# Performance work log

Measured on AMD Instinct MI355X. Metric: run time of the kernel, lower is better.

The kernel has to match this reference:

```python
import jax, jax.numpy as jnp
import numpy as np
import math

B, S, HID, NH = 4, 2048, 1024, 16
HD = HID // NH  # head dim = 64


def setup_inputs() -> dict:
    key = jax.random.key(0)
    ks = jax.random.split(key, 8)
    sc = 0.02
    return {
        "x": jax.random.normal(ks[0], (B, S, HID), dtype=jnp.float32),
        "att_mask": jnp.zeros((B, 1, 1, S), dtype=jnp.float32),
        "Wq": jax.random.normal(ks[1], (HID, HID), dtype=jnp.float32) * sc,
        "bq": jax.random.normal(ks[2], (HID,), dtype=jnp.float32) * sc,
        "Wk": jax.random.normal(ks[3], (HID, HID), dtype=jnp.float32) * sc,
        "bk": jax.random.normal(ks[4], (HID,), dtype=jnp.float32) * sc,
        "Wv": jax.random.normal(ks[5], (HID, HID), dtype=jnp.float32) * sc,
        "bv": jax.random.normal(ks[6], (HID,), dtype=jnp.float32) * sc,
    }


def reference(x, att_mask, Wq, bq, Wk, bk, Wv, bv):
    # quant_mode=False path: QuantLinear acts as a plain affine projection
    # (the running min/max stats only calibrate `scale`, which is unused in
    # the float path), and IntSoftmax reduces to a standard softmax.
    q = x @ Wq.T + bq  # [B,S,HID]
    k = x @ Wk.T + bk
    v = x @ Wv.T + bv
    # split heads: [B,S,HID] -> [B,NH,S,HD]
    q = q.reshape(B, S, NH, HD).transpose(0, 2, 1, 3)
    k = k.reshape(B, S, NH, HD).transpose(0, 2, 1, 3)
    v = v.reshape(B, S, NH, HD).transpose(0, 2, 1, 3)
    scores = jnp.einsum("bhqd,bhkd->bhqk", q, k) / math.sqrt(HD) + att_mask
    probs = jax.nn.softmax(scores, axis=-1)  # [B,NH,S,S]
    ctx = jnp.einsum("bhqk,bhkd->bhqd", probs, v)  # [B,NH,S,HD]
    return ctx.transpose(0, 2, 1, 3).reshape(B, S, HID)
```

## Files before the change

### kernel.cpp

```cpp
#include <hip/hip_runtime.h>
#include <hip/hip_bf16.h>
#include <cstdint>
#include <cstddef>

#define BB   4
#define SS   2048
#define HIDD 1024
#define NHH  16
#define HDD  64
#define MM   (BB*SS)
#define L2E  1.4426950408889634f
#define SH4  5.770780163555854f

typedef __bf16    bf16x8 __attribute__((ext_vector_type(8)));
typedef float     f32x4  __attribute__((ext_vector_type(4)));
typedef _Float16  half4  __attribute__((ext_vector_type(4)));
typedef _Float16  half8  __attribute__((ext_vector_type(8)));
typedef _Float16  half2v __attribute__((ext_vector_type(2)));
typedef unsigned  u32x4  __attribute__((ext_vector_type(4)));

__device__ __forceinline__ unsigned short f2b(float f) {
    unsigned u = __builtin_bit_cast(unsigned, f);
    return (unsigned short)((u + 0x7FFFu + ((u >> 16) & 1u)) >> 16);
}

__device__ __forceinline__ half2v pkrtz(float a, float b) {
    return __builtin_bit_cast(half2v, __builtin_amdgcn_cvt_pkrtz(a, b));
}

__device__ __forceinline__ unsigned pkrtz_u(float a, float b) {
    return __builtin_bit_cast(unsigned, __builtin_amdgcn_cvt_pkrtz(a, b));
}

__device__ __forceinline__ void gl_lds16(const void* g, void* l) {
    __builtin_amdgcn_global_load_lds(
        (const __attribute__((address_space(1))) void*)g,
        (__attribute__((address_space(3))) void*)l, 16, 0, 0);
}

#define NX4 (MM * HIDD / 4)
#define NW4 (HIDD * HIDD / 4)
__global__ __launch_bounds__(256) void cvt_all(
    const float* __restrict__ x,  const float* __restrict__ wq,
    const float* __restrict__ wk, const float* __restrict__ wv,
    unsigned short* __restrict__ xb, unsigned short* __restrict__ wb)
{
    int i = blockIdx.x * 256 + threadIdx.x;
    const float* src; unsigned short* dst; int off;
    if (i < NX4) { src = x; dst = xb; off = i; }
    else {
        int j = i - NX4;
        int w = j >> 18;
        off = j & (NW4 - 1);
        src = (w == 0) ? wq : (w == 1) ? wk : wv;
        dst = wb + (size_t)w * HIDD * HIDD;
    }
    float4 v = reinterpret_cast<const float4*>(src)[off];
    ushort4 o;
    o.x = f2b(v.x); o.y = f2b(v.y); o.z = f2b(v.z); o.w = f2b(v.w);
    reinterpret_cast<ushort4*>(dst)[off] = o;
}

__global__ __launch_bounds__(256, 3) void qkv_gemm(
    const unsigned short* __restrict__ xb,
    const unsigned short* __restrict__ wb,
    const float* __restrict__ bq, const float* __restrict__ bk, const float* __restrict__ bv,
    unsigned short* __restrict__ Qb, unsigned short* __restrict__ Kb,
    _Float16* __restrict__ Vtb)
{
    __shared__ unsigned short lA[128 * 64];
    __shared__ unsigned short lB[128 * 64];

    const int tid  = threadIdx.x;
    const int wave = tid >> 6, lane = tid & 63;
    const int lh   = lane & 15, quad = lane >> 4;
    const int l7   = lh & 7;
    const int m0   = blockIdx.x * 128;
    const int opn  = blockIdx.y;
    const int op   = opn >> 3;
    const int n0   = (opn & 7) * 128;
    const unsigned short* W = wb + (size_t)op * HIDD * HIDD;
    const float* bias = (op == 0) ? bq : (op == 1) ? bk : bv;

    f32x4 acc[4][4];
#pragma unroll
    for (int i = 0; i < 4; i++)
#pragma unroll
        for (int j = 0; j < 4; j++) acc[i][j] = f32x4{0.f, 0.f, 0.f, 0.f};

    const int wm = wave & 1, wn = wave >> 1;
    const unsigned short* srcA = (op == 2) ? lA : lB;
    const unsigned short* srcB = (op == 2) ? lB : lA;
    const int offA = (op == 2) ? wm : wn;
    const int offB = (op == 2) ? wn : wm;

    const int srow = tid >> 3;
    const int sg   = tid & 7;

    for (int k0 = 0; k0 < HIDD; k0 += 64) {
#pragma unroll
        for (int rr = 0; rr < 4; rr++) {
            const int row = srow + rr * 32;
            const int gcol = k0 + ((sg ^ (row & 7)) << 3);
            gl_lds16(&xb[(size_t)(m0 + row) * HIDD + gcol], &lA[row * 64 + sg * 8]);
            gl_lds16(&W [(size_t)(n0 + row) * HIDD + gcol], &lB[row * 64 + sg * 8]);
        }
        __syncthreads();

#pragma unroll
        for (int kk = 0; kk < 2; kk++) {
            bf16x8 aF[4], bF[4];
#pragma unroll
            for (int i = 0; i < 4; i++) {
                const int row = offA * 64 + i * 16 + lh;
                aF[i] = *reinterpret_cast<const bf16x8*>(
                    &srcA[row * 64 + (((kk * 4 + quad) ^ l7) << 3)]);
            }
#pragma unroll
            for (int j = 0; j < 4; j++) {
                const int row = offB * 64 + j * 16 + lh;
                bF[j] = *reinterpret_cast<const bf16x8*>(
                    &srcB[row * 64 + (((kk * 4 + quad) ^ l7) << 3)]);
            }
#pragma unroll
            for (int i = 0; i < 4; i++)
#pragma unroll
                for (int j = 0; j < 4; j++)
                    acc[i][j] = __builtin_amdgcn_mfma_f32_16x16x32_bf16(aF[i], bF[j], acc[i][j], 0, 0, 0);
        }
        __syncthreads();
    }

    if (op == 2) {
#pragma unroll
        for (int j = 0; j < 4; j++) {
            const int n = n0 + offB * 64 + j * 16 + lh;
            const float bvv = bias[n];
            const int h = n >> 6, d = n & 63;
#pragma unroll
            for (int i = 0; i < 4; i++) {
                const int mrow = m0 + offA * 64 + i * 16 + quad * 4;
                const int b_ = mrow >> 11, s_ = mrow & 2047;
                half2v h01 = pkrtz(acc[i][j][0] + bvv, acc[i][j][1] + bvv);
                half2v h23 = pkrtz(acc[i][j][2] + bvv, acc[i][j][3] + bvv);
                half4 hv; hv[0] = h01[0]; hv[1] = h01[1]; hv[2] = h23[0]; hv[3] = h23[1];
                size_t a = ((size_t)(b_ * NHH + h) * HDD + d) * SS + s_;
                *reinterpret_cast<half4*>(&Vtb[a]) = hv;
            }
        }
    } else {
        const float qs = (op == 0) ? (0.125f * L2E) : 1.0f;
        unsigned short* dst = (op == 0) ? Qb : Kb;
#pragma unroll
        for (int i = 0; i < 4; i++) {
            const int nb = n0 + offA * 64 + i * 16 + quad * 4;
            const float4 bb = *reinterpret_cast<const float4*>(&bias[nb]);
            const int h = nb >> 6, d = nb & 63;
#pragma unroll
            for (int j = 0; j < 4; j++) {
                const int m = m0 + offB * 64 + j * 16 + lh;
                const int b_ = m >> 11, s_ = m & 2047;
                ushort4 o;
                o.x = f2b((acc[i][j][0] + bb.x) * qs);
                o.y = f2b((acc[i][j][1] + bb.y) * qs);
                o.z = f2b((acc[i][j][2] + bb.z) * qs);
                o.w = f2b((acc[i][j][3] + bb.w) * qs);
                *reinterpret_cast<ushort4*>(
                    &dst[((size_t)(b_ * NHH + h) * SS + s_) * HDD + d]) = o;
            }
        }
    }
}

__global__ __launch_bounds__(256, 4) void attn_kernel(
    const unsigned short* __restrict__ Qb,
    const unsigned short* __restrict__ Kb,
    const _Float16* __restrict__ Vtb,
    const float* __restrict__ mask,
    float* __restrict__ out)
{
    __shared__ unsigned short lK[2][64 * 64];
    __shared__ _Float16      lV[2][64 * 64];
    __shared__ float         lmm[SS];

    const int tid  = threadIdx.x;
    const int wave = tid >> 6, lane = tid & 63;
    const int lh   = lane & 15, quad = lane >> 4;
    const int l7   = lh & 7;
    const int bh = blockIdx.x, qt = blockIdx.y;
    const int b = bh >> 4, h = bh & 15;
    const unsigned short* Qh = Qb  + (size_t)bh * SS * HDD;
    const unsigned short* Kh = Kb  + (size_t)bh * SS * HDD;
    const _Float16*       Vh = Vtb + (size_t)bh * HDD * SS;
    const float* mk = mask + (size_t)b * SS;
    const int q0 = qt * 128;

    bf16x8 qF[2][2];
#pragma unroll
    for (int i = 0; i < 2; i++)
#pragma unroll
        for (int kk = 0; kk < 2; kk++)
            qF[i][kk] = *reinterpret_cast<const bf16x8*>(
                &Qh[(size_t)(q0 + wave * 32 + i * 16 + lh) * HDD + kk * 32 + quad * 8]);

    f32x4 oacc[2][4];
#pragma unroll
    for (int i = 0; i < 2; i++)
#pragma unroll
        for (int dj = 0; dj < 4; dj++) oacc[i][dj] = f32x4{0.f, 0.f, 0.f, 0.f};
    f32x4 osum[2] = {f32x4{0.f, 0.f, 0.f, 0.f}, f32x4{0.f, 0.f, 0.f, 0.f}};

    const u32x4 one_u = {0x3C003C00u, 0x3C003C00u, 0x3C003C00u, 0x3C003C00u};
    const half8 vone  = __builtin_bit_cast(half8, one_u);

    const int srow = tid >> 3;
    const int sg   = tid & 7;

#define STAGE(KT, BUF) do {                                                     \
    const int kb_ = (KT) * 64;                                                  \
    _Pragma("unroll")                                                           \
    for (int rr = 0; rr < 2; rr++) {                                            \
        const int row = srow + rr * 32;                                         \
        const int swk = ((sg ^ ((row & 3) | ((row >> 1) & 4))) << 3);           \
        const int swv = ((sg ^ (row & 7)) << 3);                                \
        gl_lds16(&Kh[(size_t)(kb_ + row) * HDD + swk], &lK[BUF][row * 64 + sg * 8]); \
        gl_lds16(&Vh[(size_t)row * SS + kb_ + swv],    &lV[BUF][row * 64 + sg * 8]); \
    }                                                                           \
} while (0)

#define A_HALF(T, PF) do {                                                     \
    _Pragma("unroll")                                                          \
    for (int a = 0; a < 2; a++) {                                              \
        const int key = (T) * 32 + ((lh & 12) << 1) + (a << 2) + (lh & 3);     \
        const int krow = key * 64;                                             \
        bf16x8 kf0 = *reinterpret_cast<const bf16x8*>(                         \
            &lK[buf][krow + ((quad ^ l7) << 3)]);                              \
        bf16x8 kf1 = *reinterpret_cast<const bf16x8*>(                         \
            &lK[buf][krow + (((4 + quad) ^ l7) << 3)]);                        \
        const f32x4 mm = *reinterpret_cast<const f32x4*>(                      \
            &lmm[kb + (T) * 32 + quad * 8 + a * 4]);                           \
        _Pragma("unroll")                                                      \
        for (int i = 0; i < 2; i++) {                                          \
            f32x4 s = __builtin_amdgcn_mfma_f32_16x16x32_bf16(kf0, qF[i][0], mm, 0, 0, 0); \
            s = __builtin_amdgcn_mfma_f32_16x16x32_bf16(kf1, qF[i][1], s, 0, 0, 0);        \
            PF[i][a * 2 + 0] = pkrtz_u(__builtin_amdgcn_exp2f(s[0]),           \
                                       __builtin_amdgcn_exp2f(s[1]));          \
            PF[i][a * 2 + 1] = pkrtz_u(__builtin_amdgcn_exp2f(s[2]),           \
                                       __builtin_amdgcn_exp2f(s[3]));          \
        }                                                                      \
    }                                                                          \
} while (0)

#define LOADV(T, VF) do {                                                      \
    _Pragma("unroll")                                                          \
    for (int dj = 0; dj < 4; dj++)                                             \
        VF[dj] = *reinterpret_cast<const half8*>(                              \
            &lV[buf][(dj * 16 + lh) * 64 + ((((T) * 4 + quad) ^ l7) << 3)]);   \
} while (0)

#define PV_HALF(PF, VF) do {                                                   \
    __builtin_amdgcn_s_setprio(1);                                             \
    _Pragma("unroll")                                                          \
    for (int i = 0; i < 2; i++) {                                              \
        const u32x4 pu = {PF[i][0], PF[i][1], PF[i][2], PF[i][3]};             \
        const half8 pF = __builtin_bit_cast(half8, pu);                        \
        osum[i] = __builtin_amdgcn_mfma_f32_16x16x32_f16(vone, pF, osum[i], 0, 0, 0); \
        _Pragma("unroll")                                                      \
        for (int dj = 0; dj < 4; dj++)                                         \
            oacc[i][dj] = __builtin_amdgcn_mfma_f32_16x16x32_f16(              \
                VF[dj], pF, oacc[i][dj], 0, 0, 0);                             \
    }                                                                          \
    __builtin_amdgcn_s_setprio(0);                                             \
} while (0)

    unsigned pfc[2][4];
    half8    vfc[4];
#pragma unroll
    for (int i = 0; i < 2; i++)
#pragma unroll
        for (int w = 0; w < 4; w++) pfc[i][w] = 0u;
#pragma unroll
    for (int dj = 0; dj < 4; dj++)
        vfc[dj] = __builtin_bit_cast(half8, u32x4{0u, 0u, 0u, 0u});

    STAGE(0, 0);

#pragma unroll
    for (int j = 0; j < 2; j++) {
        const int idx = tid * 8 + j * 4;
        float4 m = *reinterpret_cast<const float4*>(&mk[idx]);
        float4 r;
        r.x = __builtin_fmaf(m.x, L2E, -SH4);
        r.y = __builtin_fmaf(m.y, L2E, -SH4);
        r.z = __builtin_fmaf(m.z, L2E, -SH4);
        r.w = __builtin_fmaf(m.w, L2E, -SH4);
        *reinterpret_cast<float4*>(&lmm[idx]) = r;
    }
    __syncthreads();

    for (int kt = 0; kt < SS / 64; kt++) {
        if (kt < SS / 64 - 1) STAGE(kt + 1, (kt + 1) & 1);
        const int buf = kt & 1;
        const int kb = kt * 64;

        PV_HALF(pfc, vfc);

        unsigned pf0[2][4];
        A_HALF(0, pf0);
        half8 vf0[4];
        LOADV(0, vf0);
        PV_HALF(pf0, vf0);

        A_HALF(1, pfc);
        LOADV(1, vfc);

        if (kt < SS / 64 - 1) __syncthreads();
    }
    PV_HALF(pfc, vfc);

#pragma unroll
    for (int i = 0; i < 2; i++) {
        const float rls = 1.0f / osum[i][0];
        const int q = q0 + wave * 32 + i * 16 + lh;
#pragma unroll
        for (int dj = 0; dj < 4; dj++) {
            float4 o4;
            o4.x = oacc[i][dj][0] * rls;
            o4.y = oacc[i][dj][1] * rls;
            o4.z = oacc[i][dj][2] * rls;
            o4.w = oacc[i][dj][3] * rls;
            *reinterpret_cast<float4*>(
                &out[((size_t)b * SS + q) * HIDD + h * HDD + dj * 16 + quad * 4]) = o4;
        }
    }
#undef PV_HALF
#undef LOADV
#undef A_HALF
#undef STAGE
}

extern "C" void kernel_launch(void* const* d_in, const int* in_sizes, int n_in,
                              void* d_out, int out_size, void* d_ws, size_t ws_size,
                              hipStream_t stream) {
    const float* x    = (const float*)d_in[0];
    const float* mask = (const float*)d_in[1];
    const float* Wq   = (const float*)d_in[2];
    const float* bq   = (const float*)d_in[3];
    const float* Wk   = (const float*)d_in[4];
    const float* bk   = (const float*)d_in[5];
    const float* Wv   = (const float*)d_in[6];
    const float* bv   = (const float*)d_in[7];
    float* out = (float*)d_out;
    (void)in_sizes; (void)n_in; (void)out_size; (void)ws_size;

    unsigned short* ws  = (unsigned short*)d_ws;
    unsigned short* xb  = ws;
    unsigned short* wb  = xb + (size_t)MM * HIDD;
    unsigned short* Qb  = wb + (size_t)3 * HIDD * HIDD;
    unsigned short* Kb  = Qb + (size_t)MM * HIDD;
    _Float16*       Vtb = (_Float16*)(Kb + (size_t)MM * HIDD);

    cvt_all<<<(NX4 + 3 * NW4) / 256, 256, 0, stream>>>(x, Wq, Wk, Wv, xb, wb);

    qkv_gemm<<<dim3(MM / 128, 24), 256, 0, stream>>>(xb, wb, bq, bk, bv, Qb, Kb, Vtb);

    attn_kernel<<<dim3(BB * NHH, SS / 128), 256, 0, stream>>>(Qb, Kb, Vtb, mask, out);
}
```

Baseline: 235.3 us.

## Triple-buffer QKV GEMM LDS staging with larger 256x128 tiles and 8 waves

The QKV projection GEMM moves from a 128x128 tile with 256 threads and single-buffered LDS to a 256x128 tile with 512 threads. It adds a three-stage LDS ring that prefetches two K-tiles ahead, using explicit vmcnt waits and raw barriers in place of __syncthreads. MFMA sections are wrapped in s_setprio raises. The aim is to overlap global-to-LDS loads with matrix math and to reuse each weight tile across more rows. In exchange it uses much more LDS (about 144 KB), which forces one block per CU, and the hand-placed wait counts must match the load count exactly.

Measured after the change: 254.3 us. 1.08x slower.

```diff
diff --git a/kernel.cpp b/kernel.cpp
--- a/kernel.cpp
+++ b/kernel.cpp
@@ -61,21 +61,21 @@
     reinterpret_cast<ushort4*>(dst)[off] = o;
 }
 
-__global__ __launch_bounds__(256, 3) void qkv_gemm(
+__global__ __launch_bounds__(512, 1) void qkv_gemm(
     const unsigned short* __restrict__ xb,
     const unsigned short* __restrict__ wb,
     const float* __restrict__ bq, const float* __restrict__ bk, const float* __restrict__ bv,
     unsigned short* __restrict__ Qb, unsigned short* __restrict__ Kb,
     _Float16* __restrict__ Vtb)
 {
-    __shared__ unsigned short lA[128 * 64];
-    __shared__ unsigned short lB[128 * 64];
+    __shared__ unsigned short lA[3][256 * 64];
+    __shared__ unsigned short lB[3][128 * 64];
 
     const int tid  = threadIdx.x;
     const int wave = tid >> 6, lane = tid & 63;
     const int lh   = lane & 15, quad = lane >> 4;
     const int l7   = lh & 7;
-    const int m0   = blockIdx.x * 128;
+    const int m0   = blockIdx.x * 256;
     const int opn  = blockIdx.y;
     const int op   = opn >> 3;
     const int n0   = (opn & 7) * 128;
@@ -88,48 +88,72 @@
 #pragma unroll
         for (int j = 0; j < 4; j++) acc[i][j] = f32x4{0.f, 0.f, 0.f, 0.f};
 
-    const int wm = wave & 1, wn = wave >> 1;
-    const unsigned short* srcA = (op == 2) ? lA : lB;
-    const unsigned short* srcB = (op == 2) ? lB : lA;
+    const int wm = wave & 3;
+    const int wn = wave >> 2;
     const int offA = (op == 2) ? wm : wn;
     const int offB = (op == 2) ? wn : wm;
 
     const int srow = tid >> 3;
     const int sg   = tid & 7;
 
-    for (int k0 = 0; k0 < HIDD; k0 += 64) {
-#pragma unroll
-        for (int rr = 0; rr < 4; rr++) {
-            const int row = srow + rr * 32;
-            const int gcol = k0 + ((sg ^ (row & 7)) << 3);
-            gl_lds16(&xb[(size_t)(m0 + row) * HIDD + gcol], &lA[row * 64 + sg * 8]);
-            gl_lds16(&W [(size_t)(n0 + row) * HIDD + gcol], &lB[row * 64 + sg * 8]);
-        }
-        __syncthreads();
-
-#pragma unroll
-        for (int kk = 0; kk < 2; kk++) {
+#define STG(T, BUF, H) do {                                                          \
+    const int k0_ = (T) * 64;                                                        \
+    const int rA0 = srow + ((H) ? 128 : 0);                                          \
+    const int rA1 = rA0 + 64;                                                        \
+    const int rB  = srow + ((H) ? 64 : 0);                                           \
+    gl_lds16(&xb[(size_t)(m0 + rA0) * HIDD + k0_ + ((sg ^ (rA0 & 7)) << 3)],         \
+             &lA[BUF][rA0 * 64 + sg * 8]);                                           \
+    gl_lds16(&xb[(size_t)(m0 + rA1) * HIDD + k0_ + ((sg ^ (rA1 & 7)) << 3)],         \
+             &lA[BUF][rA1 * 64 + sg * 8]);                                           \
+    gl_lds16(&W [(size_t)(n0 + rB ) * HIDD + k0_ + ((sg ^ (rB  & 7)) << 3)],         \
+             &lB[BUF][rB * 64 + sg * 8]);                                            \
+} while (0)
+
+    STG(0, 0, 0); STG(0, 0, 1);
+    STG(1, 1, 0); STG(1, 1, 1);
+    asm volatile("s_waitcnt vmcnt(6)" ::: "memory");
+    __builtin_amdgcn_s_barrier();
+
+    for (int t = 0; t < 16; ++t) {
+        const int buf  = t % 3;
+        const int nbuf = (t + 2) % 3;
+        const unsigned short* sA = (op == 2) ? lA[buf] : lB[buf];
+        const unsigned short* sB = (op == 2) ? lB[buf] : lA[buf];
+
+#pragma unroll
+        for (int kk = 0; kk < 2; ++kk) {
+            if (t + 2 < 16) STG(t + 2, nbuf, kk);
             bf16x8 aF[4], bF[4];
 #pragma unroll
-            for (int i = 0; i < 4; i++) {
-                const int row = offA * 64 + i * 16 + lh;
+            for (int i = 0; i < 4; i++)
                 aF[i] = *reinterpret_cast<const bf16x8*>(
-                    &srcA[row * 64 + (((kk * 4 + quad) ^ l7) << 3)]);
-            }
-#pragma unroll
-            for (int j = 0; j < 4; j++) {
-                const int row = offB * 64 + j * 16 + lh;
+                    &sA[(offA * 64 + i * 16 + lh) * 64 + (((kk * 4 + quad) ^ l7) << 3)]);
+#pragma unroll
+            for (int j = 0; j < 4; j++)
                 bF[j] = *reinterpret_cast<const bf16x8*>(
-                    &srcB[row * 64 + (((kk * 4 + quad) ^ l7) << 3)]);
-            }
+                    &sB[(offB * 64 + j * 16 + lh) * 64 + (((kk * 4 + quad) ^ l7) << 3)]);
+            __builtin_amdgcn_sched_barrier(0);
+            __builtin_amdgcn_s_barrier();
+            __builtin_amdgcn_s_setprio(1);
 #pragma unroll
             for (int i = 0; i < 4; i++)
 #pragma unroll
                 for (int j = 0; j < 4; j++)
                     acc[i][j] = __builtin_amdgcn_mfma_f32_16x16x32_bf16(aF[i], bF[j], acc[i][j], 0, 0, 0);
-        }
-        __syncthreads();
-    }
+            __builtin_amdgcn_s_setprio(0);
+            if (kk == 0) {
+                __builtin_amdgcn_sched_barrier(0);
+                __builtin_amdgcn_s_barrier();
+            }
+        }
+        if (t < 15) {
+            __builtin_amdgcn_sched_barrier(0);
+            if (t < 14) asm volatile("s_waitcnt vmcnt(6)" ::: "memory");
+            else        asm volatile("s_waitcnt vmcnt(0)" ::: "memory");
+            __builtin_amdgcn_s_barrier();
+        }
+    }
+#undef STG
 
     if (op == 2) {
 #pragma unroll
@@ -362,7 +386,7 @@
 
     cvt_all<<<(NX4 + 3 * NW4) / 256, 256, 0, stream>>>(x, Wq, Wk, Wv, xb, wb);
 
-    qkv_gemm<<<dim3(MM / 128, 24), 256, 0, stream>>>(xb, wb, bq, bk, bv, Qb, Kb, Vtb);
+    qkv_gemm<<<dim3(MM / 256, 24), 512, 0, stream>>>(xb, wb, bq, bk, bv, Qb, Kb, Vtb);
 
     attn_kernel<<<dim3(BB * NHH, SS / 128), 256, 0, stream>>>(Qb, Kb, Vtb, mask, out);
 }
```
